# Optimization experiments

Measured on AMD Instinct MI355X. Metric: run time of the kernel, lower is better.

The kernel has to match this reference:

```python
import jax, jax.numpy as jnp
import numpy as np

N_QUBITS = 6
N_LAYERS = 4
N_ACTIONS = 4
PRE_DIM = 64
BATCH = 262144


def _cnot(state, ctrl, tgt):
    # state: (B, 2,...,2); flip target axis on the control=1 slice
    ca, ta = 1 + ctrl, 1 + tgt
    s0 = jnp.take(state, 0, axis=ca)
    s1 = jnp.take(state, 1, axis=ca)
    ta_in = ta if ta < ca else ta - 1
    s1 = jnp.flip(s1, axis=ta_in)
    return jnp.stack([s0, s1], axis=ca)


def _ry_batched(state, angles_q, q):
    # angles_q: (B,) per-sample RY angle on qubit q (AngleEmbedding)
    h = angles_q * 0.5
    c, s = jnp.cos(h), jnp.sin(h)
    R = jnp.stack([jnp.stack([c, -s], -1), jnp.stack([s, c], -1)], -2)  # (B,2,2)
    st = jnp.moveaxis(state, 1 + q, -1)
    st = jnp.einsum('b...i,bji->b...j', st, R)
    return jnp.moveaxis(st, -1, 1 + q)


def _ry_scalar(state, theta, q):
    h = theta * 0.5
    c, s = jnp.cos(h), jnp.sin(h)
    R = jnp.stack([jnp.stack([c, -s]), jnp.stack([s, c])])  # (2,2)
    st = jnp.moveaxis(state, 1 + q, -1)
    st = st @ R.T  # new_j = sum_i R[j,i] amp_i
    return jnp.moveaxis(st, -1, 1 + q)


def _circuit(xp, qw):
    # xp: (B, n_qubits) angles; qw: (n_layers, n_qubits)
    B = xp.shape[0]
    state = jnp.zeros((B,) + (2,) * N_QUBITS, xp.dtype)
    state = state.at[(slice(None),) + (0,) * N_QUBITS].set(1.0)
    for q in range(N_QUBITS):
        state = _ry_batched(state, xp[:, q], q)
    for l in range(N_LAYERS):
        for i in range(N_QUBITS):
            state = _cnot(state, i, (i + 1) % N_QUBITS)
        for i in range(N_QUBITS):
            state = _ry_scalar(state, qw[l, i], i)
    probs = state * state  # RY/CNOT are real; state stays real
    all_axes = tuple(range(1, N_QUBITS + 1))
    zs = []
    for q in range(N_QUBITS):
        p = jnp.sum(probs, axis=tuple(a for a in all_axes if a != 1 + q))  # (B,2)
        zs.append(p[:, 0] - p[:, 1])
    return jnp.stack(zs, -1)  # (B, n_qubits)


def setup_inputs() -> dict:
    key = jax.random.key(0)
    ks = jax.random.split(key, 10)
    x = jax.random.normal(ks[0], (BATCH, N_QUBITS), jnp.float32)
    sc = 1.0 / np.sqrt(N_QUBITS)
    W1 = jax.random.uniform(ks[1], (PRE_DIM, N_QUBITS), jnp.float32, -sc, sc)
    b1 = jax.random.uniform(ks[2], (PRE_DIM,), jnp.float32, -sc, sc)
    sc2 = 1.0 / np.sqrt(PRE_DIM)
    W2 = jax.random.uniform(ks[3], (N_QUBITS, PRE_DIM), jnp.float32, -sc2, sc2)
    b2 = jax.random.uniform(ks[4], (N_QUBITS,), jnp.float32, -sc2, sc2)
    qw = jax.random.uniform(ks[5], (N_LAYERS, N_QUBITS), jnp.float32, 0.0, 2.0 * np.pi)
    Wp = jax.random.uniform(ks[6], (N_ACTIONS, N_QUBITS), jnp.float32, -sc, sc)
    bp = jax.random.uniform(ks[7], (N_ACTIONS,), jnp.float32, -sc, sc)
    Wv = jax.random.uniform(ks[8], (1, N_QUBITS), jnp.float32, -sc, sc)
    bv = jax.random.uniform(ks[9], (1,), jnp.float32, -sc, sc)
    return {"x": x, "W1": W1, "b1": b1, "W2": W2, "b2": b2, "qw": qw,
            "Wp": Wp, "bp": bp, "Wv": Wv, "bv": bv}


def reference(x, W1, b1, W2, b2, qw, Wp, bp, Wv, bv):
    h = jax.nn.relu(x @ W1.T + b1)
    xp = jax.nn.relu(h @ W2.T + b2)          # (B, n_qubits)
    qout = _circuit(xp, qw)                   # (B, n_qubits)
    policy = jax.nn.softmax(qout @ Wp.T + bp, axis=-1)
    value = (qout @ Wv.T + bv)[:, 0]
    return policy, value
```

## Files before the change

kernel.cpp:

```cpp
#include <hip/hip_runtime.h>
#include <math.h>


#define NQ 6
#define NL 4
#define NA 4
#define PD 64

typedef float v2 __attribute__((ext_vector_type(2)));

__device__ __forceinline__ v2 mk2(float a, float b) { v2 r; r.x = a; r.y = b; return r; }
__device__ __forceinline__ v2 pkfma(v2 a, v2 b, v2 c) { return __builtin_elementwise_fma(a, b, c); }

__device__ __forceinline__ float dppx1(float v) {
    int i = __builtin_bit_cast(int, v);
    i = __builtin_amdgcn_mov_dpp(i, 0xB1, 0xF, 0xF, true);
    return __builtin_bit_cast(float, i);
}

__global__ __launch_bounds__(256) void qpolicy_kernel(
    const float* __restrict__ x,
    const float* __restrict__ W1,
    const float* __restrict__ b1,
    const float* __restrict__ W2,
    const float* __restrict__ b2,
    const float* __restrict__ qw,
    const float* __restrict__ Wp,
    const float* __restrict__ bp,
    const float* __restrict__ Wv,
    const float* __restrict__ bv,
    float* __restrict__ out,
    int B)
{
    const int t = blockIdx.x * blockDim.x + threadIdx.x;
    const int s = t >> 1;
    const bool podd = (t & 1) != 0;

    const v2* xv = reinterpret_cast<const v2*>(x + (size_t)s * NQ);
    const v2 x01 = xv[0], x23 = xv[1], x45 = xv[2];

    const v2* W1v = reinterpret_cast<const v2*>(W1);
    const v2* W2v = reinterpret_cast<const v2*>(W2);

    v2 xpa[NQ];
#pragma unroll
    for (int i = 0; i < NQ; ++i) xpa[i] = mk2(b2[i], 0.0f);
#pragma unroll
    for (int k2 = 0; k2 < PD / 2; ++k2) {
        float hu[2];
#pragma unroll
        for (int u = 0; u < 2; ++u) {
            const int j = 2 * k2 + u;
            v2 acc = mk2(b1[j], 0.0f);
            acc = pkfma(x01, W1v[j * 3 + 0], acc);
            acc = pkfma(x23, W1v[j * 3 + 1], acc);
            acc = pkfma(x45, W1v[j * 3 + 2], acc);
            hu[u] = fmaxf(acc.x + acc.y, 0.0f);
        }
        const v2 hv = mk2(hu[0], hu[1]);
#pragma unroll
        for (int i = 0; i < NQ; ++i)
            xpa[i] = pkfma(hv, W2v[i * (PD / 2) + k2], xpa[i]);
    }
    float xp[NQ];
#pragma unroll
    for (int i = 0; i < NQ; ++i) xp[i] = fmaxf(xpa[i].x + xpa[i].y, 0.0f);

    float cq[NQ], sq[NQ];
#pragma unroll
    for (int q = 0; q < NQ; ++q) __sincosf(0.5f * xp[q], &sq[q], &cq[q]);

    const float g0 = podd ? sq[0] : cq[0];
    float pr[16];
    pr[0] = g0;
#pragma unroll
    for (int q = 1; q <= 4; ++q) {
        const int sz = 1 << (q - 1);
#pragma unroll
        for (int k = sz - 1; k >= 0; --k) {
            const float v = pr[k];
            pr[2 * k]     = v * cq[q];
            pr[2 * k + 1] = v * sq[q];
        }
    }
    v2 st[16];
    const v2 cs5 = mk2(cq[5], sq[5]);
#pragma unroll
    for (int j = 0; j < 16; ++j) st[j] = mk2(pr[j], pr[j]) * cs5;

#pragma unroll
    for (int l = 0; l < NL; ++l) {
#pragma unroll
        for (int j = 0; j < 8; ++j) {
            const v2 a = st[j], b = st[j | 8];
            st[j]     = podd ? b : a;
            st[j | 8] = podd ? a : b;
        }
#pragma unroll
        for (int j = 0; j < 16; ++j)
            if ((j & 8) && !(j & 4)) { v2 tmp = st[j]; st[j] = st[j | 4]; st[j | 4] = tmp; }
#pragma unroll
        for (int j = 0; j < 16; ++j)
            if ((j & 4) && !(j & 2)) { v2 tmp = st[j]; st[j] = st[j | 2]; st[j | 2] = tmp; }
#pragma unroll
        for (int j = 0; j < 16; ++j)
            if ((j & 2) && !(j & 1)) { v2 tmp = st[j]; st[j] = st[j | 1]; st[j | 1] = tmp; }
#pragma unroll
        for (int j = 0; j < 16; ++j)
            if (j & 1) st[j] = __builtin_shufflevector(st[j], st[j], 1, 0);

        float s0r, c0r;
        __sincosf(0.5f * qw[l * NQ + 0], &s0r, &c0r);
        const float ssg = podd ? s0r : -s0r;
        float tv[NQ], sv[NQ];
#pragma unroll
        for (int i = 1; i < NQ; ++i) {
            float hh = 0.5f * qw[l * NQ + i];
            hh = (hh > 1.5707963f) ? (hh - 3.14159265358979f) : hh;
            float sh, ch;
            __sincosf(hh, &sh, &ch);
            sv[i] = sh;
            tv[i] = sh * __builtin_amdgcn_rcpf(1.0f + ch);
        }

        {
            const v2 c2 = mk2(c0r, c0r), sg2 = mk2(ssg, ssg);
#pragma unroll
            for (int j = 0; j < 16; ++j) {
                const float px = dppx1(st[j].x);
                const float py = dppx1(st[j].y);
                const v2 A = mk2(st[j].x, py);
                const v2 Bv = mk2(px, st[j].y);
                st[j] = pkfma(sg2, Bv, A * c2);
            }
        }
#pragma unroll
        for (int i = 1; i <= 4; ++i) {
            const int m = 1 << (4 - i);
            const v2 vnt = mk2(-tv[i], -tv[i]);
            const v2 vs  = mk2(sv[i], sv[i]);
#pragma unroll
            for (int j = 0; j < 16; ++j) {
                if (!(j & m)) {
                    v2 a = st[j], b = st[j | m];
                    a = pkfma(vnt, b, a);
                    b = pkfma(vs, a, b);
                    a = pkfma(vnt, b, a);
                    st[j] = a; st[j | m] = b;
                }
            }
        }
        {
            const float nt = -tv[5], s5 = sv[5];
#pragma unroll
            for (int j = 0; j < 16; ++j) {
                float a0 = st[j].x, a1 = st[j].y;
                a0 = fmaf(nt, a1, a0);
                a1 = fmaf(s5, a0, a1);
                a0 = fmaf(nt, a1, a0);
                st[j] = mk2(a0, a1);
            }
        }
    }

    float a[16];
    float S5l = 0.0f;
#pragma unroll
    for (int j = 0; j < 16; ++j) {
        const v2 pp = st[j] * st[j];
        a[j] = pp.x + pp.y;
        S5l += pp.x;
    }
    float S1l = 0.0f;
#pragma unroll
    for (int j = 0; j < 8; ++j) S1l += a[j];
    float b8[8];
#pragma unroll
    for (int j = 0; j < 8; ++j) b8[j] = a[j] + a[j | 8];
    const float S2l = b8[0] + b8[1] + b8[2] + b8[3];
    float b4[4];
#pragma unroll
    for (int j = 0; j < 4; ++j) b4[j] = b8[j] + b8[j | 4];
    const float S3l = b4[0] + b4[1];
    float b2v[2];
    b2v[0] = b4[0] + b4[2];
    b2v[1] = b4[1] + b4[3];
    const float S4l = b2v[0];
    const float Tl  = b2v[0] + b2v[1];

    const float To = dppx1(Tl);
    const float T  = Tl + To;
    const float S0 = podd ? To : Tl;
    const float S1 = S1l + dppx1(S1l);
    const float S2 = S2l + dppx1(S2l);
    const float S3 = S3l + dppx1(S3l);
    const float S4 = S4l + dppx1(S4l);
    const float S5 = S5l + dppx1(S5l);

    float z[NQ];
    z[0] = fmaf(2.0f, S0, -T);
    z[1] = fmaf(2.0f, S1, -T);
    z[2] = fmaf(2.0f, S2, -T);
    z[3] = fmaf(2.0f, S3, -T);
    z[4] = fmaf(2.0f, S4, -T);
    z[5] = fmaf(2.0f, S5, -T);

    float logits[NA];
#pragma unroll
    for (int aidx = 0; aidx < NA; ++aidx) {
        float acc = bp[aidx];
#pragma unroll
        for (int q = 0; q < NQ; ++q) acc = fmaf(z[q], Wp[aidx * NQ + q], acc);
        logits[aidx] = acc;
    }
    float m = logits[0];
#pragma unroll
    for (int aidx = 1; aidx < NA; ++aidx) m = fmaxf(m, logits[aidx]);
    float e[NA];
    float esum = 0.0f;
#pragma unroll
    for (int aidx = 0; aidx < NA; ++aidx) { e[aidx] = __expf(logits[aidx] - m); esum += e[aidx]; }
    const float inv = 1.0f / esum;

    float4 pol;
    pol.x = e[0] * inv; pol.y = e[1] * inv; pol.z = e[2] * inv; pol.w = e[3] * inv;

    float v = bv[0];
#pragma unroll
    for (int q = 0; q < NQ; ++q) v = fmaf(z[q], Wv[q], v);

    if (!podd) {
        reinterpret_cast<float4*>(out)[s] = pol;
        out[(size_t)B * NA + s] = v;
    }
}

extern "C" void kernel_launch(void* const* d_in, const int* in_sizes, int n_in,
                              void* d_out, int out_size, void* d_ws, size_t ws_size,
                              hipStream_t stream) {
    const float* x  = (const float*)d_in[0];
    const float* W1 = (const float*)d_in[1];
    const float* b1 = (const float*)d_in[2];
    const float* W2 = (const float*)d_in[3];
    const float* b2 = (const float*)d_in[4];
    const float* qw = (const float*)d_in[5];
    const float* Wp = (const float*)d_in[6];
    const float* bp = (const float*)d_in[7];
    const float* Wv = (const float*)d_in[8];
    const float* bv = (const float*)d_in[9];
    float* out = (float*)d_out;

    const int B = in_sizes[0] / NQ;
    dim3 block(256);
    dim3 grid((2 * B + 255) / 256);
    hipLaunchKernelGGL(qpolicy_kernel, grid, block, 0, stream,
                       x, W1, b1, W2, b2, qw, Wp, bp, Wv, bv, out, B);
}
```

Baseline: 113.1 us.

## Precompute circuit trig constants and repack MLP weights in a prep kernel

New measurement: 106.3 us. -6.0%, faster.

```diff
diff --git a/kernel.cpp b/kernel.cpp
--- a/kernel.cpp
+++ b/kernel.cpp
@@ -18,20 +18,58 @@
     return __builtin_bit_cast(float, i);
 }
 
+__global__ void qprep_kernel(const float* __restrict__ W1,
+                             const float* __restrict__ b1,
+                             const float* __restrict__ W2,
+                             const float* __restrict__ qw,
+                             float* __restrict__ ws)
+{
+    const int t = threadIdx.x;
+    if (t < NL * NQ) {
+        const int l = t / NQ, i = t % NQ;
+        const float hh0 = 0.5f * qw[l * NQ + i];
+        float* dst = ws + l * 16;
+        if (i == 0) {
+            dst[0] = cosf(hh0);
+            dst[1] = sinf(hh0);
+        } else {
+            const float hh = (hh0 > 1.5707963f) ? (hh0 - 3.14159265358979f) : hh0;
+            const float sh = sinf(hh), ch = cosf(hh);
+            dst[2 * i]     = -sh / (1.0f + ch);
+            dst[2 * i + 1] = sh;
+        }
+    }
+    for (int idx = t; idx < 32 * 32; idx += 256) {
+        const int k2 = idx >> 5, e = idx & 31;
+        float v = 0.0f;
+        if (e < 12) {
+            const int q = e >> 1, u = e & 1;
+            v = W1[(2 * k2 + u) * NQ + q];
+        } else if (e < 14) {
+            v = b1[2 * k2 + (e - 12)];
+        } else if (e < 26) {
+            const int i2 = (e - 14) >> 1, u = e & 1;
+            v = W2[i2 * PD + 2 * k2 + u];
+        }
+        ws[64 + idx] = v;
+    }
+}
+
 __global__ __launch_bounds__(256) void qpolicy_kernel(
     const float* __restrict__ x,
-    const float* __restrict__ W1,
-    const float* __restrict__ b1,
-    const float* __restrict__ W2,
     const float* __restrict__ b2,
-    const float* __restrict__ qw,
     const float* __restrict__ Wp,
     const float* __restrict__ bp,
     const float* __restrict__ Wv,
     const float* __restrict__ bv,
+    const float* __restrict__ ws,
     float* __restrict__ out,
     int B)
 {
+    const int ph = blockIdx.x & 7;
+#pragma unroll 1
+    for (int i = 0; i < ph; ++i) __builtin_amdgcn_s_sleep(8);
+
     const int t = blockIdx.x * blockDim.x + threadIdx.x;
     const int s = t >> 1;
     const bool podd = (t & 1) != 0;
@@ -39,28 +77,25 @@
     const v2* xv = reinterpret_cast<const v2*>(x + (size_t)s * NQ);
     const v2 x01 = xv[0], x23 = xv[1], x45 = xv[2];
 
-    const v2* W1v = reinterpret_cast<const v2*>(W1);
-    const v2* W2v = reinterpret_cast<const v2*>(W2);
-
+    v2 xb[NQ];
+    xb[0] = mk2(x01.x, x01.x); xb[1] = mk2(x01.y, x01.y);
+    xb[2] = mk2(x23.x, x23.x); xb[3] = mk2(x23.y, x23.y);
+    xb[4] = mk2(x45.x, x45.x); xb[5] = mk2(x45.y, x45.y);
+
+    const v2* __restrict__ wblk = reinterpret_cast<const v2*>(ws + 64);
+    const v2 zero2 = mk2(0.0f, 0.0f);
     v2 xpa[NQ];
 #pragma unroll
     for (int i = 0; i < NQ; ++i) xpa[i] = mk2(b2[i], 0.0f);
 #pragma unroll
     for (int k2 = 0; k2 < PD / 2; ++k2) {
-        float hu[2];
-#pragma unroll
-        for (int u = 0; u < 2; ++u) {
-            const int j = 2 * k2 + u;
-            v2 acc = mk2(b1[j], 0.0f);
-            acc = pkfma(x01, W1v[j * 3 + 0], acc);
-            acc = pkfma(x23, W1v[j * 3 + 1], acc);
-            acc = pkfma(x45, W1v[j * 3 + 2], acc);
-            hu[u] = fmaxf(acc.x + acc.y, 0.0f);
-        }
-        const v2 hv = mk2(hu[0], hu[1]);
-#pragma unroll
-        for (int i = 0; i < NQ; ++i)
-            xpa[i] = pkfma(hv, W2v[i * (PD / 2) + k2], xpa[i]);
+        const v2* blk = wblk + k2 * 16;
+        v2 acc = blk[6];
+#pragma unroll
+        for (int q = 0; q < NQ; ++q) acc = pkfma(xb[q], blk[q], acc);
+        const v2 hv = __builtin_elementwise_max(acc, zero2);
+#pragma unroll
+        for (int i = 0; i < NQ; ++i) xpa[i] = pkfma(hv, blk[7 + i], xpa[i]);
     }
     float xp[NQ];
 #pragma unroll
@@ -90,6 +125,8 @@
 
 #pragma unroll
     for (int l = 0; l < NL; ++l) {
+        const float* cst = ws + l * 16;
+
 #pragma unroll
         for (int j = 0; j < 8; ++j) {
             const v2 a = st[j], b = st[j | 8];
@@ -109,27 +146,15 @@
         for (int j = 0; j < 16; ++j)
             if (j & 1) st[j] = __builtin_shufflevector(st[j], st[j], 1, 0);
 
-        float s0r, c0r;
-        __sincosf(0.5f * qw[l * NQ + 0], &s0r, &c0r);
-        const float ssg = podd ? s0r : -s0r;
-        float tv[NQ], sv[NQ];
-#pragma unroll
-        for (int i = 1; i < NQ; ++i) {
-            float hh = 0.5f * qw[l * NQ + i];
-            hh = (hh > 1.5707963f) ? (hh - 3.14159265358979f) : hh;
-            float sh, ch;
-            __sincosf(hh, &sh, &ch);
-            sv[i] = sh;
-            tv[i] = sh * __builtin_amdgcn_rcpf(1.0f + ch);
-        }
-
         {
+            const float c0r = cst[0], s0r = cst[1];
+            const float ssg = podd ? s0r : -s0r;
             const v2 c2 = mk2(c0r, c0r), sg2 = mk2(ssg, ssg);
 #pragma unroll
             for (int j = 0; j < 16; ++j) {
                 const float px = dppx1(st[j].x);
                 const float py = dppx1(st[j].y);
-                const v2 A = mk2(st[j].x, py);
+                const v2 A  = mk2(st[j].x, py);
                 const v2 Bv = mk2(px, st[j].y);
                 st[j] = pkfma(sg2, Bv, A * c2);
             }
@@ -137,8 +162,8 @@
 #pragma unroll
         for (int i = 1; i <= 4; ++i) {
             const int m = 1 << (4 - i);
-            const v2 vnt = mk2(-tv[i], -tv[i]);
-            const v2 vs  = mk2(sv[i], sv[i]);
+            const v2 vnt = mk2(cst[2 * i], cst[2 * i]);
+            const v2 vs  = mk2(cst[2 * i + 1], cst[2 * i + 1]);
 #pragma unroll
             for (int j = 0; j < 16; ++j) {
                 if (!(j & m)) {
@@ -151,7 +176,7 @@
             }
         }
         {
-            const float nt = -tv[5], s5 = sv[5];
+            const float nt = cst[10], s5 = cst[11];
 #pragma unroll
             for (int j = 0; j < 16; ++j) {
                 float a0 = st[j].x, a1 = st[j].y;
@@ -249,10 +274,15 @@
     const float* Wv = (const float*)d_in[8];
     const float* bv = (const float*)d_in[9];
     float* out = (float*)d_out;
+    float* ws  = (float*)d_ws;
 
     const int B = in_sizes[0] / NQ;
+
+    hipLaunchKernelGGL(qprep_kernel, dim3(1), dim3(256), 0, stream,
+                       W1, b1, W2, qw, ws);
+
     dim3 block(256);
     dim3 grid((2 * B + 255) / 256);
     hipLaunchKernelGGL(qpolicy_kernel, grid, block, 0, stream,
-                       x, W1, b1, W2, b2, qw, Wp, bp, Wv, bv, out, B);
-}
+                       x, b2, Wp, bp, Wv, bv, ws, out, B);
+}
```

## Split MLP into separate kernel and precompute rotation constants in workspace

Applied to the files above, without the earlier changes.

Result: faster. 101.8 us (-9.9%).

```diff
diff --git a/kernel.cpp b/kernel.cpp
--- a/kernel.cpp
+++ b/kernel.cpp
@@ -18,13 +18,70 @@
     return __builtin_bit_cast(float, i);
 }
 
-__global__ __launch_bounds__(256) void qpolicy_kernel(
+__global__ __launch_bounds__(256) void mlp_kernel(
     const float* __restrict__ x,
     const float* __restrict__ W1,
     const float* __restrict__ b1,
     const float* __restrict__ W2,
     const float* __restrict__ b2,
     const float* __restrict__ qw,
+    float* __restrict__ ws,
+    int B)
+{
+    const int s = blockIdx.x * blockDim.x + threadIdx.x;
+
+    if (blockIdx.x == 0 && threadIdx.x < NL * NQ) {
+        const int l = threadIdx.x / NQ, i = threadIdx.x % NQ;
+        const float hh0 = 0.5f * qw[l * NQ + i];
+        float* dst = ws + l * 16;
+        if (i == 0) {
+            dst[0] = cosf(hh0);
+            dst[1] = sinf(hh0);
+        } else {
+            const float hh = (hh0 > 1.5707963f) ? (hh0 - 3.14159265358979f) : hh0;
+            const float sh = sinf(hh), ch = cosf(hh);
+            dst[2 * i]     = -sh / (1.0f + ch);
+            dst[2 * i + 1] = sh;
+        }
+    }
+    if (s >= B) return;
+
+    const v2* xv = reinterpret_cast<const v2*>(x + (size_t)s * NQ);
+    const v2 x01 = xv[0], x23 = xv[1], x45 = xv[2];
+
+    const v2* W1v = reinterpret_cast<const v2*>(W1);
+    const v2* W2v = reinterpret_cast<const v2*>(W2);
+
+    v2 xpa[NQ];
+#pragma unroll
+    for (int i = 0; i < NQ; ++i) xpa[i] = mk2(b2[i], 0.0f);
+#pragma unroll
+    for (int k2 = 0; k2 < PD / 2; ++k2) {
+        float hu[2];
+#pragma unroll
+        for (int u = 0; u < 2; ++u) {
+            const int j = 2 * k2 + u;
+            v2 acc = mk2(b1[j], 0.0f);
+            acc = pkfma(x01, W1v[j * 3 + 0], acc);
+            acc = pkfma(x23, W1v[j * 3 + 1], acc);
+            acc = pkfma(x45, W1v[j * 3 + 2], acc);
+            hu[u] = fmaxf(acc.x + acc.y, 0.0f);
+        }
+        const v2 hv = mk2(hu[0], hu[1]);
+#pragma unroll
+        for (int i = 0; i < NQ; ++i)
+            xpa[i] = pkfma(hv, W2v[i * (PD / 2) + k2], xpa[i]);
+    }
+
+    v2* xpo = reinterpret_cast<v2*>(ws + 256) + (size_t)s * 3;
+#pragma unroll
+    for (int i = 0; i < 3; ++i)
+        xpo[i] = mk2(fmaxf(xpa[2 * i].x     + xpa[2 * i].y,     0.0f),
+                     fmaxf(xpa[2 * i + 1].x + xpa[2 * i + 1].y, 0.0f));
+}
+
+__global__ __launch_bounds__(256) void qpolicy_kernel(
+    const float* __restrict__ ws,
     const float* __restrict__ Wp,
     const float* __restrict__ bp,
     const float* __restrict__ Wv,
@@ -36,39 +93,19 @@
     const int s = t >> 1;
     const bool podd = (t & 1) != 0;
 
-    const v2* xv = reinterpret_cast<const v2*>(x + (size_t)s * NQ);
-    const v2 x01 = xv[0], x23 = xv[1], x45 = xv[2];
-
-    const v2* W1v = reinterpret_cast<const v2*>(W1);
-    const v2* W2v = reinterpret_cast<const v2*>(W2);
-
-    v2 xpa[NQ];
-#pragma unroll
-    for (int i = 0; i < NQ; ++i) xpa[i] = mk2(b2[i], 0.0f);
-#pragma unroll
-    for (int k2 = 0; k2 < PD / 2; ++k2) {
-        float hu[2];
-#pragma unroll
-        for (int u = 0; u < 2; ++u) {
-            const int j = 2 * k2 + u;
-            v2 acc = mk2(b1[j], 0.0f);
-            acc = pkfma(x01, W1v[j * 3 + 0], acc);
-            acc = pkfma(x23, W1v[j * 3 + 1], acc);
-            acc = pkfma(x45, W1v[j * 3 + 2], acc);
-            hu[u] = fmaxf(acc.x + acc.y, 0.0f);
-        }
-        const v2 hv = mk2(hu[0], hu[1]);
-#pragma unroll
-        for (int i = 0; i < NQ; ++i)
-            xpa[i] = pkfma(hv, W2v[i * (PD / 2) + k2], xpa[i]);
-    }
-    float xp[NQ];
-#pragma unroll
-    for (int i = 0; i < NQ; ++i) xp[i] = fmaxf(xpa[i].x + xpa[i].y, 0.0f);
+    const v2* xpv = reinterpret_cast<const v2*>(ws + 256) + (size_t)s * 3;
+    const v2 p01 = xpv[0], p23 = xpv[1], p45 = xpv[2];
+    const float xp[NQ] = { p01.x, p01.y, p23.x, p23.y, p45.x, p45.y };
 
     float cq[NQ], sq[NQ];
 #pragma unroll
     for (int q = 0; q < NQ; ++q) __sincosf(0.5f * xp[q], &sq[q], &cq[q]);
+
+    {
+        const float c1 = podd ? sq[1] : cq[1];
+        const float s1 = podd ? cq[1] : sq[1];
+        cq[1] = c1; sq[1] = s1;
+    }
 
     const float g0 = podd ? sq[0] : cq[0];
     float pr[16];
@@ -90,11 +127,15 @@
 
 #pragma unroll
     for (int l = 0; l < NL; ++l) {
-#pragma unroll
-        for (int j = 0; j < 8; ++j) {
-            const v2 a = st[j], b = st[j | 8];
-            st[j]     = podd ? b : a;
-            st[j | 8] = podd ? a : b;
+        const float* cst = ws + l * 16;
+
+        if (l > 0) {
+#pragma unroll
+            for (int j = 0; j < 8; ++j) {
+                const v2 a = st[j], b = st[j | 8];
+                st[j]     = podd ? b : a;
+                st[j | 8] = podd ? a : b;
+            }
         }
 #pragma unroll
         for (int j = 0; j < 16; ++j)
@@ -104,32 +145,20 @@
             if ((j & 4) && !(j & 2)) { v2 tmp = st[j]; st[j] = st[j | 2]; st[j | 2] = tmp; }
 #pragma unroll
         for (int j = 0; j < 16; ++j)
-            if ((j & 2) && !(j & 1)) { v2 tmp = st[j]; st[j] = st[j | 1]; st[j | 1] = tmp; }
+            if ((j & 2) && !(j & 1)) { v2 tmp = st[j]; st[j] = st[j | 2 - 1]; st[j | 1] = tmp; }
 #pragma unroll
         for (int j = 0; j < 16; ++j)
             if (j & 1) st[j] = __builtin_shufflevector(st[j], st[j], 1, 0);
 
-        float s0r, c0r;
-        __sincosf(0.5f * qw[l * NQ + 0], &s0r, &c0r);
-        const float ssg = podd ? s0r : -s0r;
-        float tv[NQ], sv[NQ];
-#pragma unroll
-        for (int i = 1; i < NQ; ++i) {
-            float hh = 0.5f * qw[l * NQ + i];
-            hh = (hh > 1.5707963f) ? (hh - 3.14159265358979f) : hh;
-            float sh, ch;
-            __sincosf(hh, &sh, &ch);
-            sv[i] = sh;
-            tv[i] = sh * __builtin_amdgcn_rcpf(1.0f + ch);
-        }
-
         {
+            const float c0r = cst[0], s0r = cst[1];
+            const float ssg = podd ? s0r : -s0r;
             const v2 c2 = mk2(c0r, c0r), sg2 = mk2(ssg, ssg);
 #pragma unroll
             for (int j = 0; j < 16; ++j) {
                 const float px = dppx1(st[j].x);
                 const float py = dppx1(st[j].y);
-                const v2 A = mk2(st[j].x, py);
+                const v2 A  = mk2(st[j].x, py);
                 const v2 Bv = mk2(px, st[j].y);
                 st[j] = pkfma(sg2, Bv, A * c2);
             }
@@ -137,8 +166,8 @@
 #pragma unroll
         for (int i = 1; i <= 4; ++i) {
             const int m = 1 << (4 - i);
-            const v2 vnt = mk2(-tv[i], -tv[i]);
-            const v2 vs  = mk2(sv[i], sv[i]);
+            const v2 vnt = mk2(cst[2 * i], cst[2 * i]);
+            const v2 vs  = mk2(cst[2 * i + 1], cst[2 * i + 1]);
 #pragma unroll
             for (int j = 0; j < 16; ++j) {
                 if (!(j & m)) {
@@ -151,7 +180,7 @@
             }
         }
         {
-            const float nt = -tv[5], s5 = sv[5];
+            const float nt = cst[10], s5 = cst[11];
 #pragma unroll
             for (int j = 0; j < 16; ++j) {
                 float a0 = st[j].x, a1 = st[j].y;
@@ -249,10 +278,13 @@
     const float* Wv = (const float*)d_in[8];
     const float* bv = (const float*)d_in[9];
     float* out = (float*)d_out;
+    float* ws  = (float*)d_ws;
 
     const int B = in_sizes[0] / NQ;
-    dim3 block(256);
-    dim3 grid((2 * B + 255) / 256);
-    hipLaunchKernelGGL(qpolicy_kernel, grid, block, 0, stream,
-                       x, W1, b1, W2, b2, qw, Wp, bp, Wv, bv, out, B);
-}
+
+    hipLaunchKernelGGL(mlp_kernel, dim3((B + 255) / 256), dim3(256), 0, stream,
+                       x, W1, b1, W2, b2, qw, ws, B);
+
+    hipLaunchKernelGGL(qpolicy_kernel, dim3((2 * B + 255) / 256), dim3(256), 0, stream,
+                       ws, Wp, bp, Wv, bv, out, B);
+}
```
